# Kernel optimization log

Measured on AMD Instinct MI355X. Metric: run time of the kernel, lower is better.

## Reference

```python
import jax, jax.numpy as jnp
import numpy as np

DIM = 256
RADIUS = 3
DIAM = 2 * RADIUS + 1          # 7
NNEIGH = DIAM * DIAM           # 49
B, H, W = 2, 64, 64
EPS_LN = 1e-6
EPS_NORM = 1e-7


def conv1x1(x, w, b):
    # x: [B,Cin,H,W], w: [Cout,Cin], b: [Cout]
    return jnp.einsum('oi,bihw->bohw', w, x) + b[None, :, None, None]


def layernorm2d(x, g, b):
    # channel-wise norm as in LayerNorm2d (mean/var over channel dim)
    u = x.mean(1, keepdims=True)
    s = ((x - u) ** 2).mean(1, keepdims=True)
    xn = (x - u) / jnp.sqrt(s + EPS_LN)
    return g[None, :, None, None] * xn + b[None, :, None, None]


def unfold_reflect(x, r):
    # torch F.unfold(pad(x, reflect, r), kernel=2r+1).reshape(B,C,D*D,H,W)
    d = 2 * r + 1
    hh, ww = x.shape[2], x.shape[3]
    xp = jnp.pad(x, ((0, 0), (0, 0), (r, r), (r, r)), mode='reflect')
    pats = [xp[:, :, i:i + hh, j:j + ww] for i in range(d) for j in range(d)]
    return jnp.stack(pats, axis=2)  # [B,C,D*D,H,W]


def setup_inputs() -> dict:
    key = jax.random.key(0)
    ks = jax.random.split(key, 20)
    sc_c = 1.0 / np.sqrt(DIM)
    sc_f = 1.0 / np.sqrt(NNEIGH + DIM)
    inp = {
        'spatial_feats': jax.random.normal(ks[0], (B, DIM, H, W), jnp.float32),
        'semantic_feats': jax.random.normal(ks[1], (B, DIM, H, W), jnp.float32),
        # range_proj: conv1x1 -> LN2d -> SiLU -> conv1x1
        'rp_w1': jax.random.normal(ks[2], (DIM, DIM), jnp.float32) * sc_c,
        'rp_b1': jnp.zeros((DIM,), jnp.float32),
        'rp_g': jnp.ones((DIM,), jnp.float32),
        'rp_be': jnp.zeros((DIM,), jnp.float32),
        'rp_w2': jax.random.normal(ks[3], (DIM, DIM), jnp.float32) * sc_c,
        'rp_b2': jnp.zeros((DIM,), jnp.float32),
        # fixup_proj: conv1x1(49+C->49) -> LN2d -> SiLU -> conv1x1(49->49)
        'fp_w1': jax.random.normal(ks[4], (NNEIGH, NNEIGH + DIM), jnp.float32) * sc_f,
        'fp_b1': jnp.zeros((NNEIGH,), jnp.float32),
        'fp_g': jnp.ones((NNEIGH,), jnp.float32),
        'fp_be': jnp.zeros((NNEIGH,), jnp.float32),
        'fp_w2': jax.random.normal(ks[5], (NNEIGH, NNEIGH), jnp.float32) * (1.0 / np.sqrt(NNEIGH)),
        'fp_b2': jnp.zeros((NNEIGH,), jnp.float32),
        # output_proj: conv1x1 -> LN2d -> conv1x1
        'op_w1': jax.random.normal(ks[6], (DIM, DIM), jnp.float32) * sc_c,
        'op_b1': jnp.zeros((DIM,), jnp.float32),
        'op_g': jnp.ones((DIM,), jnp.float32),
        'op_be': jnp.zeros((DIM,), jnp.float32),
        'op_w2': jax.random.normal(ks[7], (DIM, DIM), jnp.float32) * sc_c,
        'op_b2': jnp.zeros((DIM,), jnp.float32),
        'sigma_spatial': jnp.ones((), jnp.float32),
    }
    return inp


def reference(spatial_feats, semantic_feats,
              rp_w1, rp_b1, rp_g, rp_be, rp_w2, rp_b2,
              fp_w1, fp_b1, fp_g, fp_be, fp_w2, fp_b2,
              op_w1, op_b1, op_g, op_be, op_w2, op_b2,
              sigma_spatial):
    scale = jnp.asarray(DIM ** 0.5, spatial_feats.dtype)
    # range_proj(semantic_feats)
    px = conv1x1(semantic_feats, rp_w1, rp_b1)
    px = jax.nn.silu(layernorm2d(px, rp_g, rp_be))
    px = conv1x1(px, rp_w2, rp_b2)  # [B,C,H,W]

    # spatial (Gaussian) kernel over the window
    lin = jnp.linspace(-1.0, 1.0, DIAM)
    xg, yg = jnp.meshgrid(lin, lin, indexing='ij')
    spatial_kernel = jnp.exp(-(xg ** 2 + yg ** 2) / (2.0 * sigma_spatial ** 2))
    spatial_kernel = spatial_kernel.reshape(1, NNEIGH, 1, 1)

    # range kernel: local similarity + softmax over the 49 neighbors
    queries = unfold_reflect(px, RADIUS)                       # [B,C,N,H,W]
    sim = jnp.einsum('bcnhw,bchw->bnhw', queries, px) / scale
    range_kernel = jax.nn.softmax(sim.astype(jnp.float32), axis=1).astype(px.dtype)

    # neighborhoods of spatial features
    neighborhoods = unfold_reflect(spatial_feats, RADIUS)      # [B,C,N,H,W]

    # gated fixup correction
    ck = range_kernel * spatial_kernel                          # [B,N,H,W]
    fx = conv1x1(jnp.concatenate([ck, semantic_feats], axis=1), fp_w1, fp_b1)
    fx = jax.nn.silu(layernorm2d(fx, fp_g, fp_be))
    fx = conv1x1(fx, fp_w2, fp_b2)
    ck = ck + ck * jax.nn.sigmoid(fx)
    ck = ck / (ck.sum(1, keepdims=True) + EPS_NORM)

    # weighted neighborhood sum
    out = jnp.einsum('bcnhw,bnhw->bchw', neighborhoods, ck)

    # output_proj (note: no SiLU here, matching the module)
    out = conv1x1(out, op_w1, op_b1)
    out = layernorm2d(out, op_g, op_be)
    out = conv1x1(out, op_w2, op_b2)
    return out
```

## Files before the change

### kernel.cpp

```cpp
#include <hip/hip_runtime.h>
#include <cstdint>

#define HW 4096
#define C_ 256
#define NN 49
#define KW 305

typedef __bf16 bf16;
typedef bf16 bf16x8 __attribute__((ext_vector_type(8)));
typedef bf16 bf16x4 __attribute__((ext_vector_type(4)));
typedef bf16 bf16x2 __attribute__((ext_vector_type(2)));
typedef float f32x4 __attribute__((ext_vector_type(4)));

#define GLD16(src, dst) __builtin_amdgcn_global_load_lds( \
    (const __attribute__((address_space(1))) uint32_t*)(src), \
    (__attribute__((address_space(3))) uint32_t*)(dst), 16, 0, 0)

__device__ __forceinline__ int refl(int i) { return i < 0 ? -i : (i > 63 ? 126 - i : i); }
__device__ __forceinline__ float sigmoidf_(float x) { return 1.f / (1.f + __expf(-x)); }

__global__ __launch_bounds__(256) void setup_k(const float* __restrict__ spatial,
                                               const float* __restrict__ semantic,
                                               const float* __restrict__ rp_w1,
                                               const float* __restrict__ rp_w2,
                                               const float* __restrict__ op_w1,
                                               const float* __restrict__ op_w2,
                                               const float* __restrict__ fp_w1,
                                               const float* __restrict__ fp_w2,
                                               const float* __restrict__ sigma,
                                               bf16* __restrict__ spb, bf16* __restrict__ seb,
                                               bf16* __restrict__ wrp1, bf16* __restrict__ wrp2,
                                               bf16* __restrict__ wop1, bf16* __restrict__ wop2,
                                               float* __restrict__ w1ckg, bf16* __restrict__ w1sb,
                                               bf16* __restrict__ w2Tg, float* __restrict__ sk)
{
    __shared__ float tile[32][33];
    const int bid = blockIdx.x, t = threadIdx.x;
    if (bid < 4096) {
        int z = bid >> 10, r = bid & 1023;
        int b = z & 1;
        const float* src = (z >> 1) ? semantic : spatial;
        bf16* dst = (z >> 1) ? seb : spb;
        int p0 = (r & 127) * 32, c0 = (r >> 7) * 32;
        int tx = t & 31, ty = t >> 5;
        const float* s = src + (size_t)b * C_ * HW;
        #pragma unroll
        for (int i = 0; i < 32; i += 8)
            tile[ty + i][tx] = s[(size_t)(c0 + ty + i) * HW + p0 + tx];
        __syncthreads();
        int p = t >> 3, cq = (t & 7) * 4;
        bf16x4 o = {(bf16)tile[cq][p], (bf16)tile[cq + 1][p], (bf16)tile[cq + 2][p], (bf16)tile[cq + 3][p]};
        *(bf16x4*)&dst[((size_t)b * HW + p0 + p) * C_ + c0 + cq] = o;
        return;
    }
    int pid = bid - 4096;
    if (pid < 256) {
        const float* src = (pid < 64) ? rp_w1 : (pid < 128) ? rp_w2 : (pid < 192) ? op_w1 : op_w2;
        bf16* dst = (pid < 64) ? wrp1 : (pid < 128) ? wrp2 : (pid < 192) ? wop1 : wop2;
        int i = ((pid & 63) * 256 + t) * 4;
        f32x4 v = *(const f32x4*)&src[i];
        bf16x4 o = {(bf16)v[0], (bf16)v[1], (bf16)v[2], (bf16)v[3]};
        *(bf16x4*)&dst[i] = o;
    } else if (pid == 256) {
        if (t < NN) {
            int i = t / 7, j = t % 7;
            float xg = (i - 3) * (1.f / 3.f), yg = (j - 3) * (1.f / 3.f);
            float s = sigma[0];
            sk[t] = __expf(-(xg * xg + yg * yg) / (2.f * s * s));
        }
    } else if (pid < 270) {
        int idx = (pid - 257) * 256 + t;
        if (idx < NN * 64) {
            int k = idx >> 6, o = idx & 63;
            w1ckg[idx] = (o < NN) ? fp_w1[o * KW + k] : 0.f;
        }
    } else if (pid < 334) {
        int idx = (pid - 270) * 256 + t;
        int o = idx >> 8, c = idx & 255;
        w1sb[idx] = (o < NN) ? (bf16)fp_w1[o * KW + NN + c] : (bf16)0.f;
    } else {
        int idx = (pid - 334) * 256 + t;
        if (idx < NN * 64) {
            int k = idx >> 6, o = idx & 63;
            w2Tg[idx] = (o < NN) ? (bf16)fp_w2[o * NN + k] : (bf16)0.f;
        }
    }
}

__device__ __forceinline__ void stage_b(const bf16* __restrict__ Wp, bf16* dst, int kc, int t)
{
    const bf16* gB = Wp + (size_t)(t >> 2) * C_ + kc + (((t & 3) ^ ((t >> 3) & 3)) * 8);
    #pragma unroll
    for (int ii = 0; ii < 4; ++ii)
        GLD16(gB + (size_t)ii * 64 * C_, dst + ii * 2048 + t * 8);
}

template<bool SILU, int MODE>
__global__ __launch_bounds__(256) void conv_pair(const bf16* __restrict__ X,
                                                 const bf16* __restrict__ W1,
                                                 const float* __restrict__ b1v,
                                                 const float* __restrict__ g,
                                                 const float* __restrict__ be,
                                                 const bf16* __restrict__ W2,
                                                 const float* __restrict__ b2v,
                                                 void* __restrict__ Yv)
{
    __shared__ __align__(16) bf16 Xf[32 * 256];
    __shared__ __align__(16) bf16 Mid[32 * 256];
    __shared__ __align__(16) bf16 Bs[2][256 * 32];
    __shared__ float lnred[32][4][2];
    const int t = threadIdx.x;
    const int lane = t & 63, wc = t >> 6;
    const int l15 = lane & 15, kb = lane >> 4;
    const long q0 = (long)blockIdx.x * 32;

    {
        const int r8 = t >> 5, slot = t & 31;
        const bf16* gX = X + (q0 + r8) * C_ + ((slot ^ (r8 & 7)) * 8);
        #pragma unroll
        for (int i = 0; i < 4; ++i)
            GLD16(gX + (size_t)i * 8 * C_, &Xf[i * 2048 + t * 8]);
    }
    stage_b(W1, &Bs[0][0], 0, t);

    const int x7 = l15 & 7;
    const int bsl = (kb ^ ((l15 >> 1) & 3)) * 8;
    int boff[4];
    #pragma unroll
    for (int n = 0; n < 4; ++n)
        boff[n] = (wc * 64 + n * 16 + l15) * 32 + bsl;
    const int a0base = l15 * 256;
    const int a1base = (16 + l15) * 256;

    f32x4 acc[2][4];
    #pragma unroll
    for (int m = 0; m < 2; ++m)
        #pragma unroll
        for (int n = 0; n < 4; ++n) acc[m][n] = (f32x4){0.f, 0.f, 0.f, 0.f};

    __syncthreads();
    int cur = 0;
    #pragma unroll
    for (int ks = 0; ks < 8; ++ks) {
        if (ks < 7) stage_b(W1, &Bs[cur ^ 1][0], (ks + 1) * 32, t);
        const int ko = ((ks * 4 + kb) ^ x7) * 8;
        bf16x8 a0 = *(const bf16x8*)&Xf[a0base + ko];
        bf16x8 a1 = *(const bf16x8*)&Xf[a1base + ko];
        #pragma unroll
        for (int n = 0; n < 4; ++n) {
            bf16x8 b = *(const bf16x8*)&Bs[cur][boff[n]];
            acc[0][n] = __builtin_amdgcn_mfma_f32_16x16x32_bf16(a0, b, acc[0][n], 0, 0, 0);
            acc[1][n] = __builtin_amdgcn_mfma_f32_16x16x32_bf16(a1, b, acc[1][n], 0, 0, 0);
        }
        __syncthreads();
        cur ^= 1;
    }

    stage_b(W2, &Bs[0][0], 0, t);

    float s4[2][4], ss4[2][4];
    #pragma unroll
    for (int m = 0; m < 2; ++m)
        #pragma unroll
        for (int r = 0; r < 4; ++r) { s4[m][r] = 0.f; ss4[m][r] = 0.f; }
    #pragma unroll
    for (int n = 0; n < 4; ++n) {
        float bo = b1v[wc * 64 + n * 16 + l15];
        #pragma unroll
        for (int m = 0; m < 2; ++m)
            #pragma unroll
            for (int r = 0; r < 4; ++r) {
                float v = acc[m][n][r] + bo;
                acc[m][n][r] = v;
                s4[m][r] += v; ss4[m][r] += v * v;
            }
    }
    #pragma unroll
    for (int off = 1; off <= 8; off <<= 1)
        #pragma unroll
        for (int m = 0; m < 2; ++m)
            #pragma unroll
            for (int r = 0; r < 4; ++r) {
                s4[m][r]  += __shfl_xor(s4[m][r], off, 64);
                ss4[m][r] += __shfl_xor(ss4[m][r], off, 64);
            }
    if (l15 == 0) {
        #pragma unroll
        for (int m = 0; m < 2; ++m)
            #pragma unroll
            for (int r = 0; r < 4; ++r) {
                lnred[m * 16 + kb * 4 + r][wc][0] = s4[m][r];
                lnred[m * 16 + kb * 4 + r][wc][1] = ss4[m][r];
            }
    }
    __syncthreads();
    float mean[2][4], rstd[2][4];
    #pragma unroll
    for (int m = 0; m < 2; ++m)
        #pragma unroll
        for (int r = 0; r < 4; ++r) {
            int p = m * 16 + kb * 4 + r;
            float st  = lnred[p][0][0] + lnred[p][1][0] + lnred[p][2][0] + lnred[p][3][0];
            float sst = lnred[p][0][1] + lnred[p][1][1] + lnred[p][2][1] + lnred[p][3][1];
            mean[m][r] = st * (1.f / 256.f);
            float var = sst * (1.f / 256.f) - mean[m][r] * mean[m][r];
            rstd[m][r] = rsqrtf(var + 1e-6f);
        }
    #pragma unroll
    for (int n = 0; n < 4; ++n) {
        int ch = wc * 64 + n * 16 + l15;
        float gv = g[ch], bev = be[ch];
        #pragma unroll
        for (int m = 0; m < 2; ++m)
            #pragma unroll
            for (int r = 0; r < 4; ++r) {
                float y = (acc[m][n][r] - mean[m][r]) * rstd[m][r] * gv + bev;
                if (SILU) y *= sigmoidf_(y);
                int p = m * 16 + kb * 4 + r;
                Mid[p * 256 + (((ch >> 3) ^ (p & 7)) * 8) + (ch & 7)] = (bf16)y;
            }
    }
    __syncthreads();

    f32x4 acc2[2][4];
    #pragma unroll
    for (int m = 0; m < 2; ++m)
        #pragma unroll
        for (int n = 0; n < 4; ++n) acc2[m][n] = (f32x4){0.f, 0.f, 0.f, 0.f};
    cur = 0;
    #pragma unroll
    for (int ks = 0; ks < 8; ++ks) {
        if (ks < 7) stage_b(W2, &Bs[cur ^ 1][0], (ks + 1) * 32, t);
        const int ko = ((ks * 4 + kb) ^ x7) * 8;
        bf16x8 a0 = *(const bf16x8*)&Mid[a0base + ko];
        bf16x8 a1 = *(const bf16x8*)&Mid[a1base + ko];
        #pragma unroll
        for (int n = 0; n < 4; ++n) {
            bf16x8 b = *(const bf16x8*)&Bs[cur][boff[n]];
            acc2[0][n] = __builtin_amdgcn_mfma_f32_16x16x32_bf16(a0, b, acc2[0][n], 0, 0, 0);
            acc2[1][n] = __builtin_amdgcn_mfma_f32_16x16x32_bf16(a1, b, acc2[1][n], 0, 0, 0);
        }
        __syncthreads();
        cur ^= 1;
    }

    if constexpr (MODE == 0) {
        #pragma unroll
        for (int n = 0; n < 4; ++n) {
            int ch = wc * 64 + n * 16 + l15;
            float bo = b2v[ch];
            #pragma unroll
            for (int m = 0; m < 2; ++m)
                #pragma unroll
                for (int r = 0; r < 4; ++r)
                    Xf[(m * 16 + kb * 4 + r) * 256 + ch] = (bf16)(acc2[m][n][r] + bo);
        }
        __syncthreads();
        bf16* Y = (bf16*)Yv;
        const int p = t >> 3, cb = (t & 7) * 32;
        #pragma unroll
        for (int i = 0; i < 4; ++i) {
            bf16x8 v = *(const bf16x8*)&Xf[p * 256 + cb + i * 8];
            *(bf16x8*)&Y[(q0 + p) * C_ + cb + i * 8] = v;
        }
    } else {
        float* Y = (float*)Yv;
        const int bb = (int)(q0 >> 12);
        #pragma unroll
        for (int n = 0; n < 4; ++n) {
            int ch = wc * 64 + n * 16 + l15;
            float bo = b2v[ch];
            #pragma unroll
            for (int m = 0; m < 2; ++m) {
                int pp = (int)(q0 & 4095) + m * 16 + kb * 4;
                f32x4 val = {acc2[m][n][0] + bo, acc2[m][n][1] + bo,
                             acc2[m][n][2] + bo, acc2[m][n][3] + bo};
                *(f32x4*)&Y[((size_t)bb * C_ + ch) * HW + pp] = val;
            }
        }
    }
}

__global__ __launch_bounds__(256) void attn_k(const bf16* __restrict__ px,
                                              const bf16* __restrict__ spb,
                                              const bf16* __restrict__ seb,
                                              const bf16* __restrict__ w1sb,
                                              const float* __restrict__ w1ckg,
                                              const bf16* __restrict__ w2Tg,
                                              const float* __restrict__ b1,
                                              const float* __restrict__ b2,
                                              const float* __restrict__ g,
                                              const float* __restrict__ be,
                                              const float* __restrict__ sk,
                                              bf16* __restrict__ outb)
{
    __shared__ __align__(16) bf16 uni[112 * 256];
    __shared__ float S[112 * 17];
    __shared__ float fxs[64 * 17];
    __shared__ __align__(16) bf16 w2lT[NN * 64];
    __shared__ float ckl[16][64];
    __shared__ float hb[4][64];

    const int t = threadIdx.x, lane = t & 63, wid = t >> 6;
    const int l15 = lane & 15, kb = lane >> 4;
    const int blk = blockIdx.x;
    const int batch = blk >> 8, tt = blk & 255;
    const int h0 = (tt >> 4) * 4, w0 = (tt & 15) * 4;
    const long base = (long)batch * HW;

    {
        #pragma unroll
        for (int i = 0; i < 13; ++i) {
            int st = i * 256 + t;
            if (st < 3200) {
                int u = st >> 5, s = st & 31;
                int uy = (u * 205) >> 11, ux = u - uy * 10;
                long grow = base + refl(h0 + uy - 3) * 64 + refl(w0 + ux - 3);
                GLD16(px + grow * C_ + ((s ^ (u & 7)) * 8), &uni[u * 256 + s * 8]);
            }
        }
        GLD16(w2Tg + t * 8, &w2lT[t * 8]);
        if (t < 136) GLD16(w2Tg + (256 + t) * 8, &w2lT[(256 + t) * 8]);
    }

    const int ppy = l15 >> 2, ppx = l15 & 3;
    const int u_p = 33 + ppy * 10 + ppx;
    const int bpbase = u_p * 256, bx7 = u_p & 7;
    const long qB = base + (h0 + ppy) * 64 + (w0 + ppx);
    const bf16* bsemp = seb + qB * C_ + kb * 8;
    const int x7 = l15 & 7;

    const int tid0 = wid, tid1 = wid + 4, tid2 = wid + 8;
    const bool t1sim = (tid1 < 7);
    const bool t2valid = (tid2 < 11);
    const int a0base = (tid0 * 16 + l15) * 256;
    const int a1base = (tid1 * 16 + l15) * 256;
    const bf16* a1g = w1sb + (size_t)(((tid1 - 7) & 3) * 16 + l15) * C_ + kb * 8;
    const bf16* a2g = w1sb + (size_t)(((tid2 - 7) & 3) * 16 + l15) * C_ + kb * 8;

    f32x4 acc0 = {0.f, 0.f, 0.f, 0.f}, acc1 = {0.f, 0.f, 0.f, 0.f}, acc2 = {0.f, 0.f, 0.f, 0.f};

    __syncthreads();

    #pragma unroll
    for (int ks = 0; ks < 8; ++ks) {
        const int kg = ks * 4 + kb;
        bf16x8 bp = *(const bf16x8*)&uni[bpbase + ((kg ^ bx7) * 8)];
        bf16x8 a0 = *(const bf16x8*)&uni[a0base + ((kg ^ x7) * 8)];
        acc0 = __builtin_amdgcn_mfma_f32_16x16x32_bf16(a0, bp, acc0, 0, 0, 0);
        bf16x8 bs = *(const bf16x8*)(bsemp + ks * 32);
        bf16x8 a1;
        if (t1sim) a1 = *(const bf16x8*)&uni[a1base + ((kg ^ x7) * 8)];
        else       a1 = *(const bf16x8*)(a1g + ks * 32);
        acc1 = __builtin_amdgcn_mfma_f32_16x16x32_bf16(a1, t1sim ? bp : bs, acc1, 0, 0, 0);
        if (t2valid) {
            bf16x8 a2 = *(const bf16x8*)(a2g + ks * 32);
            acc2 = __builtin_amdgcn_mfma_f32_16x16x32_bf16(a2, bs, acc2, 0, 0, 0);
        }
    }
    {
        float* dst = &S[(tid0 * 16 + kb * 4) * 17 + l15];
        dst[0] = acc0[0]; dst[17] = acc0[1]; dst[34] = acc0[2]; dst[51] = acc0[3];
    }
    if (t1sim) {
        float* dst = &S[(tid1 * 16 + kb * 4) * 17 + l15];
        dst[0] = acc1[0]; dst[17] = acc1[1]; dst[34] = acc1[2]; dst[51] = acc1[3];
    } else {
        float* dst = &fxs[(kb * 4) * 17 + l15];
        dst[0] = acc1[0]; dst[17] = acc1[1]; dst[34] = acc1[2]; dst[51] = acc1[3];
    }
    if (t2valid) {
        float* dst = &fxs[((tid2 - 7) * 16 + kb * 4) * 17 + l15];
        dst[0] = acc2[0]; dst[17] = acc2[1]; dst[34] = acc2[2]; dst[51] = acc2[3];
    }
    __syncthreads();

    #pragma unroll
    for (int i = 0; i < 13; ++i) {
        int st = i * 256 + t;
        if (st < 3200) {
            int u = st >> 5, s = st & 31;
            int uy = (u * 205) >> 11, ux = u - uy * 10;
            long grow = base + refl(h0 + uy - 3) * 64 + refl(w0 + ux - 3);
            GLD16(spb + grow * C_ + ((s ^ (u & 7)) * 8), &uni[u * 256 + s * 8]);
        }
    }

    float w1r[NN];
    #pragma unroll
    for (int k = 0; k < NN; ++k) w1r[k] = w1ckg[k * 64 + lane];

    const float skv = (lane < NN) ? sk[lane] : 0.f;
    const int nn_ = (lane < NN) ? lane : 0;
    const int dy = nn_ / 7, dx = nn_ % 7;
    #pragma unroll
    for (int j = 0; j < 4; ++j) {
        int p = wid * 4 + j, py = p >> 2, px4 = p & 3;
        int u = (py + dy) * 10 + px4 + dx;
        float sval = (lane < NN) ? S[u * 17 + p] * 0.0625f : -1e30f;
        float mx = sval;
        #pragma unroll
        for (int off = 32; off; off >>= 1) mx = fmaxf(mx, __shfl_xor(mx, off, 64));
        float ev = (lane < NN) ? __expf(sval - mx) : 0.f;
        float ssum = ev;
        #pragma unroll
        for (int off = 32; off; off >>= 1) ssum += __shfl_xor(ssum, off, 64);
        ckl[p][lane] = (lane < NN) ? (ev / ssum) * skv : 0.f;
    }

    const float bo  = (lane < NN) ? b1[lane] : 0.f;
    const float gl  = (lane < NN) ? g[lane] : 0.f;
    const float bel = (lane < NN) ? be[lane] : 0.f;
    const float b2l = (lane < NN) ? b2[lane] : 0.f;
    #pragma unroll
    for (int j = 0; j < 4; ++j) {
        int p = wid * 4 + j;
        float fx = fxs[lane * 17 + p] + bo;
        #pragma unroll 7
        for (int k = 0; k < NN; ++k) fx += w1r[k] * ckl[p][k];
        float s = fx, ss = fx * fx;
        #pragma unroll
        for (int off = 32; off; off >>= 1) {
            s  += __shfl_xor(s, off, 64);
            ss += __shfl_xor(ss, off, 64);
        }
        float mean = s * (1.f / 49.f);
        float var  = ss * (1.f / 49.f) - mean * mean;
        float rstd = rsqrtf(var + 1e-6f);
        float hv = 0.f;
        if (lane < NN) {
            float xn = (fx - mean) * rstd * gl + bel;
            hv = xn * sigmoidf_(xn);
        }
        hb[wid][lane] = hv;
        float ckv = 0.f;
        if (lane < NN) {
            float fx2 = b2l;
            #pragma unroll 7
            for (int k = 0; k < NN; ++k) fx2 += (float)w2lT[k * 64 + lane] * hb[wid][k];
            ckv = ckl[p][lane] * (1.f + sigmoidf_(fx2));
        }
        float tot = ckv;
        #pragma unroll
        for (int off = 32; off; off >>= 1) tot += __shfl_xor(tot, off, 64);
        ckl[p][lane] = (lane < NN) ? ckv / (tot + 1e-7f) : 0.f;
    }
    __syncthreads();

    const int hh_ = lane >> 5, l31 = lane & 31;
    #pragma unroll
    for (int jj = 0; jj < 2; ++jj) {
        int p = wid * 4 + jj * 2 + hh_;
        int py = p >> 2, px4 = p & 3;
        long q = base + (h0 + py) * 64 + (w0 + px4);
        int ub = py * 10 + px4;
        float a[8];
        #pragma unroll
        for (int e = 0; e < 8; ++e) a[e] = 0.f;
        for (int dyy = 0; dyy < 7; ++dyy) {
            #pragma unroll
            for (int dxx = 0; dxx < 7; ++dxx) {
                int u = ub + dyy * 10 + dxx;
                float cv = ckl[p][dyy * 7 + dxx];
                bf16x8 v = *(const bf16x8*)&uni[u * 256 + ((l31 ^ (u & 7)) * 8)];
                #pragma unroll
                for (int e = 0; e < 8; ++e) a[e] += cv * (float)v[e];
            }
        }
        bf16x8 ov;
        #pragma unroll
        for (int e = 0; e < 8; ++e) ov[e] = (bf16)a[e];
        *(bf16x8*)&outb[q * C_ + l31 * 8] = ov;
    }
}

extern "C" void kernel_launch(void* const* d_in, const int* in_sizes, int n_in,
                              void* d_out, int out_size, void* d_ws, size_t ws_size,
                              hipStream_t stream)
{
    const float* spatial  = (const float*)d_in[0];
    const float* semantic = (const float*)d_in[1];
    const float* rp_w1 = (const float*)d_in[2];
    const float* rp_b1 = (const float*)d_in[3];
    const float* rp_g  = (const float*)d_in[4];
    const float* rp_be = (const float*)d_in[5];
    const float* rp_w2 = (const float*)d_in[6];
    const float* rp_b2 = (const float*)d_in[7];
    const float* fp_w1 = (const float*)d_in[8];
    const float* fp_b1 = (const float*)d_in[9];
    const float* fp_g  = (const float*)d_in[10];
    const float* fp_be = (const float*)d_in[11];
    const float* fp_w2 = (const float*)d_in[12];
    const float* fp_b2 = (const float*)d_in[13];
    const float* op_w1 = (const float*)d_in[14];
    const float* op_b1 = (const float*)d_in[15];
    const float* op_g  = (const float*)d_in[16];
    const float* op_be = (const float*)d_in[17];
    const float* op_w2 = (const float*)d_in[18];
    const float* op_b2 = (const float*)d_in[19];
    const float* sigma = (const float*)d_in[20];

    const size_t NPX = 2 * (size_t)HW;
    float* ws = (float*)d_ws;
    float* sk    = ws;
    float* w1ckg = sk + 64;
    bf16* bfbase = (bf16*)(w1ckg + 3200);
    bf16* spb = bfbase;
    bf16* seb = spb + NPX * C_;
    bf16* t0  = seb + NPX * C_;
    bf16* t1  = t0  + NPX * C_;
    bf16* wrp1 = t1 + NPX * C_;
    bf16* wrp2 = wrp1 + C_ * C_;
    bf16* wop1 = wrp2 + C_ * C_;
    bf16* wop2 = wop1 + C_ * C_;
    bf16* w1sb = wop2 + C_ * C_;
    bf16* w2Tg = w1sb + 64 * C_;

    setup_k<<<4443, 256, 0, stream>>>(spatial, semantic, rp_w1, rp_w2, op_w1, op_w2,
                                      fp_w1, fp_w2, sigma,
                                      spb, seb, wrp1, wrp2, wop1, wop2,
                                      w1ckg, w1sb, w2Tg, sk);

    conv_pair<true, 0><<<256, 256, 0, stream>>>(seb, wrp1, rp_b1, rp_g, rp_be, wrp2, rp_b2, t1);

    attn_k<<<512, 256, 0, stream>>>(t1, spb, seb, w1sb, w1ckg, w2Tg, fp_b1, fp_b2,
                                    fp_g, fp_be, sk, t0);

    conv_pair<false, 1><<<256, 256, 0, stream>>>(t0, wop1, op_b1, op_g, op_be, wop2, op_b2, d_out);
}
```

Baseline: 73.45 us.

## Double attn_k block to 512 threads and redistribute MFMA tiles across 8 waves

The attention kernel now runs 8 waves per block instead of 4. The 11 MFMA tile jobs (7 similarity tiles and 4 fixup tiles) are spread so each wave does at most two, and each wave handles two pixels instead of four in the softmax, fixup and weighted-sum phases. The weighted-sum loop also loads all seven neighbor vectors of a row before accumulating, to get more LDS loads in flight. This aims to cut per-wave serial work and raise latency hiding, at the cost of more registers per block (w1r[49] plus v[7]) under the 512-thread launch bound, which may limit occupancy.

```diff
diff --git a/kernel.cpp b/kernel.cpp
--- a/kernel.cpp
+++ b/kernel.cpp
@@ -281,7 +281,7 @@
     }
 }
 
-__global__ __launch_bounds__(256) void attn_k(const bf16* __restrict__ px,
+__global__ __launch_bounds__(512) void attn_k(const bf16* __restrict__ px,
                                               const bf16* __restrict__ spb,
                                               const bf16* __restrict__ seb,
                                               const bf16* __restrict__ w1sb,
@@ -299,7 +299,7 @@
     __shared__ float fxs[64 * 17];
     __shared__ __align__(16) bf16 w2lT[NN * 64];
     __shared__ float ckl[16][64];
-    __shared__ float hb[4][64];
+    __shared__ float hb[8][64];
 
     const int t = threadIdx.x, lane = t & 63, wid = t >> 6;
     const int l15 = lane & 15, kb = lane >> 4;
@@ -308,20 +308,17 @@
     const int h0 = (tt >> 4) * 4, w0 = (tt & 15) * 4;
     const long base = (long)batch * HW;
 
-    {
-        #pragma unroll
-        for (int i = 0; i < 13; ++i) {
-            int st = i * 256 + t;
-            if (st < 3200) {
-                int u = st >> 5, s = st & 31;
-                int uy = (u * 205) >> 11, ux = u - uy * 10;
-                long grow = base + refl(h0 + uy - 3) * 64 + refl(w0 + ux - 3);
-                GLD16(px + grow * C_ + ((s ^ (u & 7)) * 8), &uni[u * 256 + s * 8]);
-            }
-        }
-        GLD16(w2Tg + t * 8, &w2lT[t * 8]);
-        if (t < 136) GLD16(w2Tg + (256 + t) * 8, &w2lT[(256 + t) * 8]);
-    }
+    #pragma unroll
+    for (int i = 0; i < 7; ++i) {
+        int st = i * 512 + t;
+        if (st < 3200) {
+            int u = st >> 5, s = st & 31;
+            int uy = (u * 205) >> 11, ux = u - uy * 10;
+            long grow = base + refl(h0 + uy - 3) * 64 + refl(w0 + ux - 3);
+            GLD16(px + grow * C_ + ((s ^ (u & 7)) * 8), &uni[u * 256 + s * 8]);
+        }
+    }
+    if (t < 392) GLD16(w2Tg + t * 8, &w2lT[t * 8]);
 
     const int ppy = l15 >> 2, ppx = l15 & 3;
     const int u_p = 33 + ppy * 10 + ppx;
@@ -330,15 +327,14 @@
     const bf16* bsemp = seb + qB * C_ + kb * 8;
     const int x7 = l15 & 7;
 
-    const int tid0 = wid, tid1 = wid + 4, tid2 = wid + 8;
-    const bool t1sim = (tid1 < 7);
-    const bool t2valid = (tid2 < 11);
+    const int tid0 = wid;
+    const bool t0sim = (tid0 < 7);
+    const bool t1valid = (wid < 3);
     const int a0base = (tid0 * 16 + l15) * 256;
-    const int a1base = (tid1 * 16 + l15) * 256;
-    const bf16* a1g = w1sb + (size_t)(((tid1 - 7) & 3) * 16 + l15) * C_ + kb * 8;
-    const bf16* a2g = w1sb + (size_t)(((tid2 - 7) & 3) * 16 + l15) * C_ + kb * 8;
-
-    f32x4 acc0 = {0.f, 0.f, 0.f, 0.f}, acc1 = {0.f, 0.f, 0.f, 0.f}, acc2 = {0.f, 0.f, 0.f, 0.f};
+    const bf16* a0g = w1sb + (size_t)l15 * C_ + kb * 8;
+    const bf16* a1g = w1sb + (size_t)((wid + 1) * 16 + l15) * C_ + kb * 8;
+
+    f32x4 acc0 = {0.f, 0.f, 0.f, 0.f}, acc1 = {0.f, 0.f, 0.f, 0.f};
 
     __syncthreads();
 
@@ -346,38 +342,32 @@
     for (int ks = 0; ks < 8; ++ks) {
         const int kg = ks * 4 + kb;
         bf16x8 bp = *(const bf16x8*)&uni[bpbase + ((kg ^ bx7) * 8)];
-        bf16x8 a0 = *(const bf16x8*)&uni[a0base + ((kg ^ x7) * 8)];
-        acc0 = __builtin_amdgcn_mfma_f32_16x16x32_bf16(a0, bp, acc0, 0, 0, 0);
         bf16x8 bs = *(const bf16x8*)(bsemp + ks * 32);
-        bf16x8 a1;
-        if (t1sim) a1 = *(const bf16x8*)&uni[a1base + ((kg ^ x7) * 8)];
-        else       a1 = *(const bf16x8*)(a1g + ks * 32);
-        acc1 = __builtin_amdgcn_mfma_f32_16x16x32_bf16(a1, t1sim ? bp : bs, acc1, 0, 0, 0);
-        if (t2valid) {
-            bf16x8 a2 = *(const bf16x8*)(a2g + ks * 32);
-            acc2 = __builtin_amdgcn_mfma_f32_16x16x32_bf16(a2, bs, acc2, 0, 0, 0);
-        }
-    }
-    {
+        bf16x8 a0;
+        if (t0sim) a0 = *(const bf16x8*)&uni[a0base + ((kg ^ x7) * 8)];
+        else       a0 = *(const bf16x8*)(a0g + ks * 32);
+        acc0 = __builtin_amdgcn_mfma_f32_16x16x32_bf16(a0, t0sim ? bp : bs, acc0, 0, 0, 0);
+        if (t1valid) {
+            bf16x8 a1 = *(const bf16x8*)(a1g + ks * 32);
+            acc1 = __builtin_amdgcn_mfma_f32_16x16x32_bf16(a1, bs, acc1, 0, 0, 0);
+        }
+    }
+    if (t0sim) {
         float* dst = &S[(tid0 * 16 + kb * 4) * 17 + l15];
         dst[0] = acc0[0]; dst[17] = acc0[1]; dst[34] = acc0[2]; dst[51] = acc0[3];
-    }
-    if (t1sim) {
-        float* dst = &S[(tid1 * 16 + kb * 4) * 17 + l15];
-        dst[0] = acc1[0]; dst[17] = acc1[1]; dst[34] = acc1[2]; dst[51] = acc1[3];
     } else {
         float* dst = &fxs[(kb * 4) * 17 + l15];
+        dst[0] = acc0[0]; dst[17] = acc0[1]; dst[34] = acc0[2]; dst[51] = acc0[3];
+    }
+    if (t1valid) {
+        float* dst = &fxs[((wid + 1) * 16 + kb * 4) * 17 + l15];
         dst[0] = acc1[0]; dst[17] = acc1[1]; dst[34] = acc1[2]; dst[51] = acc1[3];
     }
-    if (t2valid) {
-        float* dst = &fxs[((tid2 - 7) * 16 + kb * 4) * 17 + l15];
-        dst[0] = acc2[0]; dst[17] = acc2[1]; dst[34] = acc2[2]; dst[51] = acc2[3];
-    }
     __syncthreads();
 
     #pragma unroll
-    for (int i = 0; i < 13; ++i) {
-        int st = i * 256 + t;
+    for (int i = 0; i < 7; ++i) {
+        int st = i * 512 + t;
         if (st < 3200) {
             int u = st >> 5, s = st & 31;
             int uy = (u * 205) >> 11, ux = u - uy * 10;
@@ -394,8 +384,8 @@
     const int nn_ = (lane < NN) ? lane : 0;
     const int dy = nn_ / 7, dx = nn_ % 7;
     #pragma unroll
-    for (int j = 0; j < 4; ++j) {
-        int p = wid * 4 + j, py = p >> 2, px4 = p & 3;
+    for (int j = 0; j < 2; ++j) {
+        int p = wid * 2 + j, py = p >> 2, px4 = p & 3;
         int u = (py + dy) * 10 + px4 + dx;
         float sval = (lane < NN) ? S[u * 17 + p] * 0.0625f : -1e30f;
         float mx = sval;
@@ -413,8 +403,8 @@
     const float bel = (lane < NN) ? be[lane] : 0.f;
     const float b2l = (lane < NN) ? b2[lane] : 0.f;
     #pragma unroll
-    for (int j = 0; j < 4; ++j) {
-        int p = wid * 4 + j;
+    for (int j = 0; j < 2; ++j) {
+        int p = wid * 2 + j;
         float fx = fxs[lane * 17 + p] + bo;
         #pragma unroll 7
         for (int k = 0; k < NN; ++k) fx += w1r[k] * ckl[p][k];
@@ -447,10 +437,9 @@
     }
     __syncthreads();
 
-    const int hh_ = lane >> 5, l31 = lane & 31;
-    #pragma unroll
-    for (int jj = 0; jj < 2; ++jj) {
-        int p = wid * 4 + jj * 2 + hh_;
+    const int l31 = lane & 31;
+    {
+        int p = wid * 2 + (lane >> 5);
         int py = p >> 2, px4 = p & 3;
         long q = base + (h0 + py) * 64 + (w0 + px4);
         int ub = py * 10 + px4;
@@ -458,13 +447,17 @@
         #pragma unroll
         for (int e = 0; e < 8; ++e) a[e] = 0.f;
         for (int dyy = 0; dyy < 7; ++dyy) {
+            bf16x8 v[7];
             #pragma unroll
             for (int dxx = 0; dxx < 7; ++dxx) {
                 int u = ub + dyy * 10 + dxx;
+                v[dxx] = *(const bf16x8*)&uni[u * 256 + ((l31 ^ (u & 7)) * 8)];
+            }
+            #pragma unroll
+            for (int dxx = 0; dxx < 7; ++dxx) {
                 float cv = ckl[p][dyy * 7 + dxx];
-                bf16x8 v = *(const bf16x8*)&uni[u * 256 + ((l31 ^ (u & 7)) * 8)];
                 #pragma unroll
-                for (int e = 0; e < 8; ++e) a[e] += cv * (float)v[e];
+                for (int e = 0; e < 8; ++e) a[e] += cv * (float)v[dxx][e];
             }
         }
         bf16x8 ov;
@@ -523,7 +516,7 @@
 
     conv_pair<true, 0><<<256, 256, 0, stream>>>(seb, wrp1, rp_b1, rp_g, rp_be, wrp2, rp_b2, t1);
 
-    attn_k<<<512, 256, 0, stream>>>(t1, spb, seb, w1sb, w1ckg, w2Tg, fp_b1, fp_b2,
+    attn_k<<<512, 512, 0, stream>>>(t1, spb, seb, w1sb, w1ckg, w2Tg, fp_b1, fp_b2,
                                     fp_g, fp_be, sk, t0);
 
     conv_pair<false, 1><<<256, 256, 0, stream>>>(t0, wop1, op_b1, op_g, op_be, wop2, op_b2, d_out);
```

After: 79.54 us. 8.3% more time.

## Read similarity operands from global, stage fixup weights as bf16 in LDS

Applied to the files above, without the earlier changes.

The attention kernel no longer stages the 10x10 px halo into shared memory before the similarity MFMAs. Each wave now reads its A and B rows straight from global memory, and the shared tile shrinks from 112 to 100 rows. The fixup conv1x1 weights for the kernel channels become bf16 and live in LDS instead of a 49-float register array, which is meant to cut register pressure and raise occupancy. The small matvecs are split into two accumulators, and the final weighted sum batches seven LDS loads per row to expose more parallelism. The trade-offs are more uncoalesced global reads per MFMA step and slightly lower weight precision.

```diff
diff --git a/kernel.cpp b/kernel.cpp
--- a/kernel.cpp
+++ b/kernel.cpp
@@ -31,7 +31,7 @@
                                                bf16* __restrict__ spb, bf16* __restrict__ seb,
                                                bf16* __restrict__ wrp1, bf16* __restrict__ wrp2,
                                                bf16* __restrict__ wop1, bf16* __restrict__ wop2,
-                                               float* __restrict__ w1ckg, bf16* __restrict__ w1sb,
+                                               bf16* __restrict__ w1ckb, bf16* __restrict__ w1sb,
                                                bf16* __restrict__ w2Tg, float* __restrict__ sk)
 {
     __shared__ float tile[32][33];
@@ -72,7 +72,7 @@
         int idx = (pid - 257) * 256 + t;
         if (idx < NN * 64) {
             int k = idx >> 6, o = idx & 63;
-            w1ckg[idx] = (o < NN) ? fp_w1[o * KW + k] : 0.f;
+            w1ckb[idx] = (o < NN) ? (bf16)fp_w1[o * KW + k] : (bf16)0.f;
         }
     } else if (pid < 334) {
         int idx = (pid - 270) * 256 + t;
@@ -285,7 +285,7 @@
                                               const bf16* __restrict__ spb,
                                               const bf16* __restrict__ seb,
                                               const bf16* __restrict__ w1sb,
-                                              const float* __restrict__ w1ckg,
+                                              const bf16* __restrict__ w1ckb,
                                               const bf16* __restrict__ w2Tg,
                                               const float* __restrict__ b1,
                                               const float* __restrict__ b2,
@@ -294,10 +294,11 @@
                                               const float* __restrict__ sk,
                                               bf16* __restrict__ outb)
 {
-    __shared__ __align__(16) bf16 uni[112 * 256];
+    __shared__ __align__(16) bf16 uni[100 * 256];
     __shared__ float S[112 * 17];
     __shared__ float fxs[64 * 17];
     __shared__ __align__(16) bf16 w2lT[NN * 64];
+    __shared__ __align__(16) bf16 w1lT[NN * 64];
     __shared__ float ckl[16][64];
     __shared__ float hb[4][64];
 
@@ -308,70 +309,63 @@
     const int h0 = (tt >> 4) * 4, w0 = (tt & 15) * 4;
     const long base = (long)batch * HW;
 
-    {
-        #pragma unroll
-        for (int i = 0; i < 13; ++i) {
-            int st = i * 256 + t;
-            if (st < 3200) {
-                int u = st >> 5, s = st & 31;
-                int uy = (u * 205) >> 11, ux = u - uy * 10;
-                long grow = base + refl(h0 + uy - 3) * 64 + refl(w0 + ux - 3);
-                GLD16(px + grow * C_ + ((s ^ (u & 7)) * 8), &uni[u * 256 + s * 8]);
-            }
-        }
-        GLD16(w2Tg + t * 8, &w2lT[t * 8]);
-        if (t < 136) GLD16(w2Tg + (256 + t) * 8, &w2lT[(256 + t) * 8]);
+    const float bo  = (lane < NN) ? b1[lane] : 0.f;
+    const float gl  = (lane < NN) ? g[lane] : 0.f;
+    const float bel = (lane < NN) ? be[lane] : 0.f;
+    const float b2l = (lane < NN) ? b2[lane] : 0.f;
+    const float skv = (lane < NN) ? sk[lane] : 0.f;
+    const int nn_ = (lane < NN) ? lane : 0;
+    const int dy = nn_ / 7, dx = nn_ % 7;
+
+    for (int i = t; i < 392; i += 256) {
+        GLD16(w2Tg + (size_t)i * 8, &w2lT[i * 8]);
+        GLD16(w1ckb + (size_t)i * 8, &w1lT[i * 8]);
     }
 
     const int ppy = l15 >> 2, ppx = l15 & 3;
-    const int u_p = 33 + ppy * 10 + ppx;
-    const int bpbase = u_p * 256, bx7 = u_p & 7;
     const long qB = base + (h0 + ppy) * 64 + (w0 + ppx);
+    const bf16* bpxp = px + qB * C_ + kb * 8;
     const bf16* bsemp = seb + qB * C_ + kb * 8;
-    const int x7 = l15 & 7;
-
-    const int tid0 = wid, tid1 = wid + 4, tid2 = wid + 8;
-    const bool t1sim = (tid1 < 7);
-    const bool t2valid = (tid2 < 11);
-    const int a0base = (tid0 * 16 + l15) * 256;
-    const int a1base = (tid1 * 16 + l15) * 256;
-    const bf16* a1g = w1sb + (size_t)(((tid1 - 7) & 3) * 16 + l15) * C_ + kb * 8;
-    const bf16* a2g = w1sb + (size_t)(((tid2 - 7) & 3) * 16 + l15) * C_ + kb * 8;
-
-    f32x4 acc0 = {0.f, 0.f, 0.f, 0.f}, acc1 = {0.f, 0.f, 0.f, 0.f}, acc2 = {0.f, 0.f, 0.f, 0.f};
-
-    __syncthreads();
+
+    bool valid[3], ispx[3];
+    const bf16* arow[3];
+    #pragma unroll
+    for (int j = 0; j < 3; ++j) {
+        int tid = wid + 4 * j;
+        valid[j] = tid < 11;
+        ispx[j] = tid < 7;
+        int u = tid * 16 + l15;
+        int uy = (u * 205) >> 11, ux = u - uy * 10;
+        long grow = (u < 100) ? base + refl(h0 + uy - 3) * 64 + refl(w0 + ux - 3) : base;
+        int o = ((tid - 7) & 3) * 16 + l15;
+        arow[j] = ispx[j] ? (px + grow * C_ + kb * 8)
+                          : (w1sb + (size_t)o * C_ + kb * 8);
+    }
+
+    f32x4 acc[3];
+    #pragma unroll
+    for (int j = 0; j < 3; ++j) acc[j] = (f32x4){0.f, 0.f, 0.f, 0.f};
 
     #pragma unroll
     for (int ks = 0; ks < 8; ++ks) {
-        const int kg = ks * 4 + kb;
-        bf16x8 bp = *(const bf16x8*)&uni[bpbase + ((kg ^ bx7) * 8)];
-        bf16x8 a0 = *(const bf16x8*)&uni[a0base + ((kg ^ x7) * 8)];
-        acc0 = __builtin_amdgcn_mfma_f32_16x16x32_bf16(a0, bp, acc0, 0, 0, 0);
+        bf16x8 bp = *(const bf16x8*)(bpxp + ks * 32);
         bf16x8 bs = *(const bf16x8*)(bsemp + ks * 32);
-        bf16x8 a1;
-        if (t1sim) a1 = *(const bf16x8*)&uni[a1base + ((kg ^ x7) * 8)];
-        else       a1 = *(const bf16x8*)(a1g + ks * 32);
-        acc1 = __builtin_amdgcn_mfma_f32_16x16x32_bf16(a1, t1sim ? bp : bs, acc1, 0, 0, 0);
-        if (t2valid) {
-            bf16x8 a2 = *(const bf16x8*)(a2g + ks * 32);
-            acc2 = __builtin_amdgcn_mfma_f32_16x16x32_bf16(a2, bs, acc2, 0, 0, 0);
-        }
-    }
-    {
-        float* dst = &S[(tid0 * 16 + kb * 4) * 17 + l15];
-        dst[0] = acc0[0]; dst[17] = acc0[1]; dst[34] = acc0[2]; dst[51] = acc0[3];
-    }
-    if (t1sim) {
-        float* dst = &S[(tid1 * 16 + kb * 4) * 17 + l15];
-        dst[0] = acc1[0]; dst[17] = acc1[1]; dst[34] = acc1[2]; dst[51] = acc1[3];
-    } else {
-        float* dst = &fxs[(kb * 4) * 17 + l15];
-        dst[0] = acc1[0]; dst[17] = acc1[1]; dst[34] = acc1[2]; dst[51] = acc1[3];
-    }
-    if (t2valid) {
-        float* dst = &fxs[((tid2 - 7) * 16 + kb * 4) * 17 + l15];
-        dst[0] = acc2[0]; dst[17] = acc2[1]; dst[34] = acc2[2]; dst[51] = acc2[3];
+        #pragma unroll
+        for (int j = 0; j < 3; ++j) {
+            if (valid[j]) {
+                bf16x8 a = *(const bf16x8*)(arow[j] + ks * 32);
+                acc[j] = __builtin_amdgcn_mfma_f32_16x16x32_bf16(a, ispx[j] ? bp : bs, acc[j], 0, 0, 0);
+            }
+        }
+    }
+    #pragma unroll
+    for (int j = 0; j < 3; ++j) {
+        if (valid[j]) {
+            int tid = wid + 4 * j;
+            float* dst = ispx[j] ? &S[(tid * 16 + kb * 4) * 17 + l15]
+                                 : &fxs[(((tid - 7) * 16) + kb * 4) * 17 + l15];
+            dst[0] = acc[j][0]; dst[17] = acc[j][1]; dst[34] = acc[j][2]; dst[51] = acc[j][3];
+        }
     }
     __syncthreads();
 
@@ -386,13 +380,6 @@
         }
     }
 
-    float w1r[NN];
-    #pragma unroll
-    for (int k = 0; k < NN; ++k) w1r[k] = w1ckg[k * 64 + lane];
-
-    const float skv = (lane < NN) ? sk[lane] : 0.f;
-    const int nn_ = (lane < NN) ? lane : 0;
-    const int dy = nn_ / 7, dx = nn_ % 7;
     #pragma unroll
     for (int j = 0; j < 4; ++j) {
         int p = wid * 4 + j, py = p >> 2, px4 = p & 3;
@@ -408,16 +395,17 @@
         ckl[p][lane] = (lane < NN) ? (ev / ssum) * skv : 0.f;
     }
 
-    const float bo  = (lane < NN) ? b1[lane] : 0.f;
-    const float gl  = (lane < NN) ? g[lane] : 0.f;
-    const float bel = (lane < NN) ? be[lane] : 0.f;
-    const float b2l = (lane < NN) ? b2[lane] : 0.f;
     #pragma unroll
     for (int j = 0; j < 4; ++j) {
         int p = wid * 4 + j;
-        float fx = fxs[lane * 17 + p] + bo;
-        #pragma unroll 7
-        for (int k = 0; k < NN; ++k) fx += w1r[k] * ckl[p][k];
+        float fxa = 0.f, fxb = 0.f;
+        #pragma unroll
+        for (int k = 0; k < 48; k += 2) {
+            fxa += (float)w1lT[k * 64 + lane] * ckl[p][k];
+            fxb += (float)w1lT[(k + 1) * 64 + lane] * ckl[p][k + 1];
+        }
+        fxa += (float)w1lT[48 * 64 + lane] * ckl[p][48];
+        float fx = fxs[lane * 17 + p] + bo + fxa + fxb;
         float s = fx, ss = fx * fx;
         #pragma unroll
         for (int off = 32; off; off >>= 1) {
@@ -435,10 +423,14 @@
         hb[wid][lane] = hv;
         float ckv = 0.f;
         if (lane < NN) {
-            float fx2 = b2l;
-            #pragma unroll 7
-            for (int k = 0; k < NN; ++k) fx2 += (float)w2lT[k * 64 + lane] * hb[wid][k];
-            ckv = ckl[p][lane] * (1.f + sigmoidf_(fx2));
+            float ca = 0.f, cb = 0.f;
+            #pragma unroll
+            for (int k = 0; k < 48; k += 2) {
+                ca += (float)w2lT[k * 64 + lane] * hb[wid][k];
+                cb += (float)w2lT[(k + 1) * 64 + lane] * hb[wid][k + 1];
+            }
+            ca += (float)w2lT[48 * 64 + lane] * hb[wid][48];
+            ckv = ckl[p][lane] * (1.f + sigmoidf_(b2l + ca + cb));
         }
         float tot = ckv;
         #pragma unroll
@@ -447,10 +439,10 @@
     }
     __syncthreads();
 
-    const int hh_ = lane >> 5, l31 = lane & 31;
+    const int l31 = lane & 31;
     #pragma unroll
     for (int jj = 0; jj < 2; ++jj) {
-        int p = wid * 4 + jj * 2 + hh_;
+        int p = wid * 4 + jj * 2 + (lane >> 5);
         int py = p >> 2, px4 = p & 3;
         long q = base + (h0 + py) * 64 + (w0 + px4);
         int ub = py * 10 + px4;
@@ -458,13 +450,17 @@
         #pragma unroll
         for (int e = 0; e < 8; ++e) a[e] = 0.f;
         for (int dyy = 0; dyy < 7; ++dyy) {
+            bf16x8 v[7];
             #pragma unroll
             for (int dxx = 0; dxx < 7; ++dxx) {
                 int u = ub + dyy * 10 + dxx;
+                v[dxx] = *(const bf16x8*)&uni[u * 256 + ((l31 ^ (u & 7)) * 8)];
+            }
+            #pragma unroll
+            for (int dxx = 0; dxx < 7; ++dxx) {
                 float cv = ckl[p][dyy * 7 + dxx];
-                bf16x8 v = *(const bf16x8*)&uni[u * 256 + ((l31 ^ (u & 7)) * 8)];
                 #pragma unroll
-                for (int e = 0; e < 8; ++e) a[e] += cv * (float)v[e];
+                for (int e = 0; e < 8; ++e) a[e] += cv * (float)v[dxx][e];
             }
         }
         bf16x8 ov;
@@ -503,8 +499,7 @@
     const size_t NPX = 2 * (size_t)HW;
     float* ws = (float*)d_ws;
     float* sk    = ws;
-    float* w1ckg = sk + 64;
-    bf16* bfbase = (bf16*)(w1ckg + 3200);
+    bf16* bfbase = (bf16*)(sk + 64);
     bf16* spb = bfbase;
     bf16* seb = spb + NPX * C_;
     bf16* t0  = seb + NPX * C_;
@@ -515,15 +510,16 @@
     bf16* wop2 = wop1 + C_ * C_;
     bf16* w1sb = wop2 + C_ * C_;
     bf16* w2Tg = w1sb + 64 * C_;
+    bf16* w1ckb = w2Tg + 3200;
 
     setup_k<<<4443, 256, 0, stream>>>(spatial, semantic, rp_w1, rp_w2, op_w1, op_w2,
                                       fp_w1, fp_w2, sigma,
                                       spb, seb, wrp1, wrp2, wop1, wop2,
-                                      w1ckg, w1sb, w2Tg, sk);
+                                      w1ckb, w1sb, w2Tg, sk);
 
     conv_pair<true, 0><<<256, 256, 0, stream>>>(seb, wrp1, rp_b1, rp_g, rp_be, wrp2, rp_b2, t1);
 
-    attn_k<<<512, 256, 0, stream>>>(t1, spb, seb, w1sb, w1ckg, w2Tg, fp_b1, fp_b2,
+    attn_k<<<512, 256, 0, stream>>>(t1, spb, seb, w1sb, w1ckb, w2Tg, fp_b1, fp_b2,
                                     fp_g, fp_be, sk, t0);
 
     conv_pair<false, 1><<<256, 256, 0, stream>>>(t0, wop1, op_b1, op_g, op_be, wop2, op_b2, d_out);
```

Result: faster. 68.15 us (-7.2%).
